# Kernel tuning notes

Measured on AMD Instinct MI355X. Metric: run time of the kernel, lower is better.

Reference implementation:

```python
import jax, jax.numpy as jnp
import numpy as np

B, To, Tw, D = 96, 50, 40, 512


def setup_inputs() -> dict:
    key = jax.random.key(0)
    ko, kw = jax.random.split(key)
    o = jax.random.normal(ko, (B, To, D), dtype=jnp.float32)
    w = jax.random.normal(kw, (B, Tw, D), dtype=jnp.float32)
    return {"o": o, "w": w}


def reference(o, w):
    # o: (Bo, To, D) box features; w: (Bw, Tw, D) caption word features.
    # fo/fw are KVIdentity => Ko=Vo=o, Kw=Vw=w.
    d = o.shape[-1]
    scale = 1.0 / jnp.sqrt(jnp.asarray(d, dtype=o.dtype))
    # cross-batch attention scores: (Bw, Bo, Tw, To)
    att = jnp.einsum('wtd,bod->wbto', w, o) * scale
    att = jax.nn.softmax(att, axis=3)           # softmax over To (boxes)
    # attended object values: (Bw, Bo, Tw, D)
    att_vo = jnp.einsum('wbto,bod->wbtd', att, o)
    # word-object compatibility logits: (Bw, Bo, Tw)
    logits = jnp.einsum('wbtd,wtd->wbt', att_vo, w)
    logp = jax.nn.log_softmax(logits, axis=1)    # contrast over Bo
    per_pair = jnp.mean(logp, axis=2)            # (Bw, Bo)
    loss = -jnp.mean(jnp.diagonal(per_pair))
    return loss
```

## Files before the change

### kernel.cpp

```cpp
#include <hip/hip_runtime.h>
#include <cstdint>
#include <cstddef>

typedef unsigned short u16;
typedef __attribute__((ext_vector_type(8))) short short8;
typedef __attribute__((ext_vector_type(8))) unsigned short u16x8;
typedef __attribute__((ext_vector_type(4))) float f32x4;

#define NB   96
#define TO   50
#define TW   40
#define DD   512
#define MROWS (NB*TW)
#define BM   128
#define BK   32
#define NKC  (DD/BK)

#define WBF_OFF   0u
#define OBF_OFF   (MROWS*DD*2u)
#define LOG_OFF   (OBF_OFF + NB*TO*DD*2u)
#define ZB_OFF    (LOG_OFF + MROWS*NB*4u)

__device__ __forceinline__ u16 f2bf(float f) {
  unsigned int u = __builtin_bit_cast(unsigned int, f);
  u += 0x7fffu + ((u >> 16) & 1u);
  return (u16)(u >> 16);
}

__device__ __forceinline__ void gload16(const void* g, void* l) {
  __builtin_amdgcn_global_load_lds(
      (__attribute__((address_space(1))) unsigned int*)(g),
      (__attribute__((address_space(3))) unsigned int*)(l), 16, 0, 0);
}

__global__ void k_convert(const float* __restrict__ o, const float* __restrict__ w,
                          u16* __restrict__ obf, u16* __restrict__ wbf,
                          u16* __restrict__ zbuf, float* __restrict__ out) {
  const int stride = gridDim.x * blockDim.x;
  const int tid0 = blockIdx.x * blockDim.x + threadIdx.x;
  const int no8 = NB*TO*DD/8;
  const int nw8 = NB*TW*DD/8;
  for (int i = tid0; i < no8; i += stride) {
    const float4* s = (const float4*)o + (size_t)i*2;
    float4 a = s[0], b = s[1];
    u16x8 r = { f2bf(a.x), f2bf(a.y), f2bf(a.z), f2bf(a.w),
                f2bf(b.x), f2bf(b.y), f2bf(b.z), f2bf(b.w) };
    *(u16x8*)(obf + (size_t)i*8) = r;
  }
  for (int i = tid0; i < nw8; i += stride) {
    const float4* s = (const float4*)w + (size_t)i*2;
    float4 a = s[0], b = s[1];
    u16x8 r = { f2bf(a.x), f2bf(a.y), f2bf(a.z), f2bf(a.w),
                f2bf(b.x), f2bf(b.y), f2bf(b.z), f2bf(b.w) };
    *(u16x8*)(wbf + (size_t)i*8) = r;
  }
  if (tid0 < 16) {
    u16x8 z = {0,0,0,0,0,0,0,0};
    *(u16x8*)(zbuf + tid0*8) = z;
  }
  if (tid0 == 0) out[0] = 0.f;
}

__global__ void __launch_bounds__(256) k_main(
    const u16* __restrict__ wbf, const u16* __restrict__ obf,
    const u16* __restrict__ zbuf, float* __restrict__ logits) {
  __shared__ u16 ldsA[2][BM*BK];
  __shared__ u16 ldsB[2][BM*BK];
  const int tid  = threadIdx.x;
  const int lane = tid & 63;
  const int wid  = tid >> 6;
  const int r0   = blockIdx.y * BM;
  const int ob0  = blockIdx.x * 2;

  const u16* gA[2];
  const u16* gB[2];
  bool realB[2];
  #pragma unroll
  for (int i = 0; i < 2; ++i) {
    int c   = i*256 + tid;
    int row = c >> 2;
    int kc8 = (c & 3) * 8;
    gA[i] = wbf + (size_t)(r0 + row) * DD + kc8;
    int ob = ob0 + (row >> 6);
    int oo = row & 63;
    realB[i] = (oo < TO);
    gB[i] = realB[i] ? (obf + ((size_t)ob * TO + oo) * DD + kc8) : zbuf;
  }
  const int ldst = (wid * 64) * 8;

  auto stage = [&](int buf, int k0) {
    #pragma unroll
    for (int i = 0; i < 2; ++i) {
      gload16(gA[i] + k0, &ldsA[buf][i*2048 + ldst]);
      gload16(realB[i] ? gB[i] + k0 : gB[i], &ldsB[buf][i*2048 + ldst]);
    }
  };

  const int wr   = (wid >> 1) * 64;
  const int wc   = (wid & 1) * 64;
  const int lrow = lane & 15;
  const int lk   = (lane >> 4) * 8;

  f32x4 zero4 = {0.f, 0.f, 0.f, 0.f};
  f32x4 acc[4][4];
  #pragma unroll
  for (int mi = 0; mi < 4; ++mi)
    #pragma unroll
    for (int ni = 0; ni < 4; ++ni) acc[mi][ni] = zero4;

  stage(0, 0);
  for (int kc = 0; kc < NKC; ++kc) {
    const int cur = kc & 1;
    __syncthreads();
    if (kc + 1 < NKC) stage(cur ^ 1, (kc + 1) * BK);
    short8 af[4], bfr[4];
    #pragma unroll
    for (int mi = 0; mi < 4; ++mi)
      af[mi] = *(const short8*)&ldsA[cur][(wr + mi*16 + lrow) * BK + lk];
    #pragma unroll
    for (int ni = 0; ni < 4; ++ni)
      bfr[ni] = *(const short8*)&ldsB[cur][(wc + ni*16 + lrow) * BK + lk];
    #pragma unroll
    for (int mi = 0; mi < 4; ++mi)
      #pragma unroll
      for (int ni = 0; ni < 4; ++ni)
        acc[mi][ni] = __builtin_amdgcn_mfma_f32_16x16x32_bf16(
            af[mi], bfr[ni], acc[mi][ni], 0, 0, 0);
  }

  const float scale = 0.04419417382415922f;
  const int ob = ob0 + (wid & 1);
  #pragma unroll
  for (int mi = 0; mi < 4; ++mi) {
    #pragma unroll
    for (int q = 0; q < 4; ++q) {
      float v0 = acc[mi][0][q], v1 = acc[mi][1][q],
            v2 = acc[mi][2][q], v3 = acc[mi][3][q];
      float m = fmaxf(fmaxf(v0, v1), v2);
      if (lrow < 2) m = fmaxf(m, v3);
      #pragma unroll
      for (int d = 1; d < 16; d <<= 1) m = fmaxf(m, __shfl_xor(m, d));
      float p0 = __expf((v0 - m) * scale);
      float p1 = __expf((v1 - m) * scale);
      float p2 = __expf((v2 - m) * scale);
      float den = p0 + p1 + p2;
      float num = p0*v0 + p1*v1 + p2*v2;
      if (lrow < 2) {
        float p3 = __expf((v3 - m) * scale);
        den += p3; num += p3*v3;
      }
      #pragma unroll
      for (int d = 1; d < 16; d <<= 1) {
        den += __shfl_xor(den, d);
        num += __shfl_xor(num, d);
      }
      if (lrow == 0) {
        int row = r0 + wr + mi*16 + (lane >> 4)*4 + q;
        logits[(size_t)row * NB + ob] = num / den;
      }
    }
  }
}

__global__ void __launch_bounds__(512) k_lse(
    const float* __restrict__ logits, float* __restrict__ out) {
  __shared__ float red[8];
  const int tid  = threadIdx.x;
  const int lane = tid & 63;
  const int wid  = tid >> 6;
  const int gw   = blockIdx.x * 8 + wid;
  float acc = 0.f;
  #pragma unroll
  for (int i = 0; i < 8; ++i) {
    const int row = gw * 8 + i;
    const float* base = logits + (size_t)row * NB;
    float v0 = base[lane];
    float v1 = (lane < NB - 64) ? base[64 + lane] : -1e30f;
    float m = fmaxf(v0, v1);
    #pragma unroll
    for (int d = 1; d < 64; d <<= 1) m = fmaxf(m, __shfl_xor(m, d));
    float den = __expf(v0 - m) + ((lane < NB - 64) ? __expf(v1 - m) : 0.f);
    #pragma unroll
    for (int d = 1; d < 64; d <<= 1) den += __shfl_xor(den, d);
    if (lane == 0) {
      const int wb = row / TW;
      acc += base[wb] - m - __logf(den);
    }
  }
  if (lane == 0) red[wid] = acc;
  __syncthreads();
  if (tid == 0) {
    float s = red[0] + red[1] + red[2] + red[3]
            + red[4] + red[5] + red[6] + red[7];
    atomicAdd(out, s * (-1.0f / (float)MROWS));
  }
}

extern "C" void kernel_launch(void* const* d_in, const int* in_sizes, int n_in,
                              void* d_out, int out_size, void* d_ws, size_t ws_size,
                              hipStream_t stream) {
  const float* o = (const float*)d_in[0];
  const float* w = (const float*)d_in[1];
  char* ws = (char*)d_ws;
  u16*    wbf     = (u16*)(ws + WBF_OFF);
  u16*    obf     = (u16*)(ws + OBF_OFF);
  float*  logits  = (float*)(ws + LOG_OFF);
  u16*    zbuf    = (u16*)(ws + ZB_OFF);

  k_convert<<<1200, 256, 0, stream>>>(o, w, obf, wbf, zbuf, (float*)d_out);
  dim3 g1(NB/2, MROWS/BM);
  k_main<<<g1, 256, 0, stream>>>(wbf, obf, zbuf, logits);
  k_lse<<<60, 512, 0, stream>>>(logits, (float*)d_out);
}
```

Baseline: 115.6 us.

## Load MFMA operands directly from global into double-buffered registers, bypassing LDS

The GEMM kernel no longer stages A and B tiles through shared memory with global_load_lds and per-iteration __syncthreads. Each wave now reads its own bf16 fragments straight from global memory into registers, prefetching the next K chunk while the current one feeds the MFMAs, and the K loop is fully unrolled. This removes the LDS traffic and block-wide barriers. In exchange, waves that share rows issue duplicate global loads that rely on the cache, the access pattern is less coalesced, and only one K step of prefetch is available to hide load latency. The zero buffer is enlarged so that padded B columns can advance through all K offsets.

Result: slower. 163.6 us (+41.6%).

```diff
diff --git a/kernel.cpp b/kernel.cpp
--- a/kernel.cpp
+++ b/kernel.cpp
@@ -25,12 +25,6 @@
   unsigned int u = __builtin_bit_cast(unsigned int, f);
   u += 0x7fffu + ((u >> 16) & 1u);
   return (u16)(u >> 16);
-}
-
-__device__ __forceinline__ void gload16(const void* g, void* l) {
-  __builtin_amdgcn_global_load_lds(
-      (__attribute__((address_space(1))) unsigned int*)(g),
-      (__attribute__((address_space(3))) unsigned int*)(l), 16, 0, 0);
 }
 
 __global__ void k_convert(const float* __restrict__ o, const float* __restrict__ w,
@@ -54,7 +48,7 @@
                 f2bf(b.x), f2bf(b.y), f2bf(b.z), f2bf(b.w) };
     *(u16x8*)(wbf + (size_t)i*8) = r;
   }
-  if (tid0 < 16) {
+  if (tid0 < 64) {
     u16x8 z = {0,0,0,0,0,0,0,0};
     *(u16x8*)(zbuf + tid0*8) = z;
   }
@@ -64,42 +58,29 @@
 __global__ void __launch_bounds__(256) k_main(
     const u16* __restrict__ wbf, const u16* __restrict__ obf,
     const u16* __restrict__ zbuf, float* __restrict__ logits) {
-  __shared__ u16 ldsA[2][BM*BK];
-  __shared__ u16 ldsB[2][BM*BK];
   const int tid  = threadIdx.x;
   const int lane = tid & 63;
   const int wid  = tid >> 6;
   const int r0   = blockIdx.y * BM;
   const int ob0  = blockIdx.x * 2;
 
-  const u16* gA[2];
-  const u16* gB[2];
-  bool realB[2];
-  #pragma unroll
-  for (int i = 0; i < 2; ++i) {
-    int c   = i*256 + tid;
-    int row = c >> 2;
-    int kc8 = (c & 3) * 8;
-    gA[i] = wbf + (size_t)(r0 + row) * DD + kc8;
-    int ob = ob0 + (row >> 6);
-    int oo = row & 63;
-    realB[i] = (oo < TO);
-    gB[i] = realB[i] ? (obf + ((size_t)ob * TO + oo) * DD + kc8) : zbuf;
-  }
-  const int ldst = (wid * 64) * 8;
-
-  auto stage = [&](int buf, int k0) {
-    #pragma unroll
-    for (int i = 0; i < 2; ++i) {
-      gload16(gA[i] + k0, &ldsA[buf][i*2048 + ldst]);
-      gload16(realB[i] ? gB[i] + k0 : gB[i], &ldsB[buf][i*2048 + ldst]);
-    }
-  };
-
-  const int wr   = (wid >> 1) * 64;
-  const int wc   = (wid & 1) * 64;
-  const int lrow = lane & 15;
-  const int lk   = (lane >> 4) * 8;
+  const int wr    = (wid >> 1) * 64;
+  const int wc    = (wid & 1) * 64;
+  const int lrow  = lane & 15;
+  const int lk8   = (lane >> 4) * 8;
+  const int ob    = ob0 + (wid & 1);
+
+  const u16* pA[4];
+  const u16* pB[4];
+  #pragma unroll
+  for (int mi = 0; mi < 4; ++mi)
+    pA[mi] = wbf + (size_t)(r0 + wr + mi*16 + lrow) * DD + lk8;
+  #pragma unroll
+  for (int ni = 0; ni < 4; ++ni) {
+    int col = ni*16 + lrow;
+    pB[ni] = (col < TO) ? (obf + ((size_t)ob * TO + col) * DD + lk8)
+                        : (zbuf + lk8);
+  }
 
   f32x4 zero4 = {0.f, 0.f, 0.f, 0.f};
   f32x4 acc[4][4];
@@ -108,28 +89,33 @@
     #pragma unroll
     for (int ni = 0; ni < 4; ++ni) acc[mi][ni] = zero4;
 
-  stage(0, 0);
+  short8 af[2][4], bf[2][4];
+  #pragma unroll
+  for (int mi = 0; mi < 4; ++mi) af[0][mi] = *(const short8*)(pA[mi]);
+  #pragma unroll
+  for (int ni = 0; ni < 4; ++ni) bf[0][ni] = *(const short8*)(pB[ni]);
+
+  #pragma unroll
   for (int kc = 0; kc < NKC; ++kc) {
-    const int cur = kc & 1;
-    __syncthreads();
-    if (kc + 1 < NKC) stage(cur ^ 1, (kc + 1) * BK);
-    short8 af[4], bfr[4];
-    #pragma unroll
-    for (int mi = 0; mi < 4; ++mi)
-      af[mi] = *(const short8*)&ldsA[cur][(wr + mi*16 + lrow) * BK + lk];
-    #pragma unroll
-    for (int ni = 0; ni < 4; ++ni)
-      bfr[ni] = *(const short8*)&ldsB[cur][(wc + ni*16 + lrow) * BK + lk];
+    const int cur = kc & 1, nxt = cur ^ 1;
+    if (kc + 1 < NKC) {
+      const int koff = (kc + 1) * BK;
+      #pragma unroll
+      for (int mi = 0; mi < 4; ++mi)
+        af[nxt][mi] = *(const short8*)(pA[mi] + koff);
+      #pragma unroll
+      for (int ni = 0; ni < 4; ++ni)
+        bf[nxt][ni] = *(const short8*)(pB[ni] + koff);
+    }
     #pragma unroll
     for (int mi = 0; mi < 4; ++mi)
       #pragma unroll
       for (int ni = 0; ni < 4; ++ni)
         acc[mi][ni] = __builtin_amdgcn_mfma_f32_16x16x32_bf16(
-            af[mi], bfr[ni], acc[mi][ni], 0, 0, 0);
+            af[cur][mi], bf[cur][ni], acc[mi][ni], 0, 0, 0);
   }
 
   const float scale = 0.04419417382415922f;
-  const int ob = ob0 + (wid & 1);
   #pragma unroll
   for (int mi = 0; mi < 4; ++mi) {
     #pragma unroll
```
